# Kernel tuning notes

Measured on AMD Instinct MI355X. Metric: run time of the kernel, lower is better.

Reference implementation:

```python
import jax, jax.numpy as jnp
import numpy as np

MEAN = jnp.array([0.4488, 0.4371, 0.404], dtype=jnp.float32)
PS, PM, PL = 1e-4, 2e-4, 3e-4  # per-branch time costs ps/pm/pl
PATCH = 32
FACTOR = 4
GROUPS = 4


def _conv(x, w, b, pad, groups=1):
    y = jax.lax.conv_general_dilated(x, w, (1, 1), [(pad, pad), (pad, pad)],
                                     dimension_numbers=('NCHW', 'OIHW', 'NCHW'),
                                     feature_group_count=groups)
    return y + b[None, :, None, None]


def _block(x, w1, b1, w2, b2):
    # residual grouped-conv Block(channels, group=4)
    y = jax.nn.relu(_conv(x, w1, b1, 1, groups=GROUPS))
    return x + _conv(y, w2, b2, 1, groups=GROUPS)


def _pixel_shuffle(x, r):
    B, C, H, W = x.shape
    x = x.reshape(B, C // (r * r), r, r, H, W)
    return x.transpose(0, 1, 4, 2, 5, 3).reshape(B, C // (r * r), H * r, W * r)


def setup_inputs() -> dict:
    key = jax.random.key(0)
    ks = jax.random.split(key, 20)
    def W(i, shape, fan):
        return jax.random.normal(ks[i], shape, jnp.float32) * (fan ** -0.5)
    Z = lambda c: jnp.zeros((c,), jnp.float32)
    return {
        'x': jax.random.uniform(ks[0], (4, 3, 160, 160), dtype=jnp.float32),
        'tl': jnp.full((1,), 0.1, jnp.float32),
        'tr': jnp.full((1,), 0.1, jnp.float32),
        'iicm_w': W(1, (12, 3, 3, 3), 27), 'iicm_b': Z(12),
        'conv4_w': W(2, (64, 12, 3, 3), 108), 'conv4_b': Z(64),
        'b1_w1': W(3, (64, 16, 3, 3), 144), 'b1_b1': Z(64),
        'b1_w2': W(4, (64, 16, 3, 3), 144), 'b1_b2': Z(64),
        'c1_w': W(5, (64, 128, 1, 1), 128), 'c1_b': Z(64),
        'b2_w1': W(6, (64, 16, 3, 3), 144), 'b2_b1': Z(64),
        'b2_w2': W(7, (64, 16, 3, 3), 144), 'b2_b2': Z(64),
        'c2_w': W(8, (64, 192, 1, 1), 192), 'c2_b': Z(64),
        'b3_w1': W(9, (64, 16, 3, 3), 144), 'b3_b1': Z(64),
        'b3_w2': W(10, (64, 16, 3, 3), 144), 'b3_b2': Z(64),
        'c3_w': W(11, (64, 256, 1, 1), 256), 'c3_b': Z(64),
        'marm_w': W(12, (64, 67, 3, 3), 603), 'marm_b': Z(64),
        'up1_w': W(13, (256, 64, 3, 3), 576), 'up1_b': Z(256),
        'up2_w': W(14, (256, 64, 3, 3), 576), 'up2_b': Z(256),
        'upc_w': W(15, (3, 64, 3, 3), 576), 'upc_b': Z(3),
    }


def reference(x, tl, tr, iicm_w, iicm_b, conv4_w, conv4_b,
              b1_w1, b1_b1, b1_w2, b1_b2, c1_w, c1_b,
              b2_w1, b2_b1, b2_w2, b2_b2, c2_w, c2_b,
              b3_w1, b3_b1, b3_w2, b3_b2, c3_w, c3_b,
              marm_w, marm_b, up1_w, up1_b, up2_w, up2_b, upc_w, upc_b):
    # ----- sub_mean -----
    x0 = x - MEAN[None, :, None, None]
    B, C, H, W = x0.shape
    hp, wp = H // PATCH, W // PATCH
    N = B * hp * wp
    # ----- decompsition_img: tile into 32x32 patches -----
    p = x0.reshape(B, C, hp, PATCH, wp, PATCH).transpose(0, 2, 4, 1, 3, 5)
    p = p.reshape(N, C, PATCH, PATCH)
    # ----- IICM: feature extraction + per-patch difficulty score ssza -----
    f = jax.nn.relu(_conv(p, iicm_w, iicm_b, 1))          # [N,12,32,32]
    ssza = jnp.mean(jnp.abs(f), axis=(1, 2, 3))           # [N]
    f = _conv(f, conv4_w, conv4_b, 1)                     # [N,64,32,32]
    # ----- branch depth 1 -----
    b1o = _block(f, b1_w1, b1_b1, b1_w2, b1_b2)
    c1o = jnp.concatenate([f, b1o], axis=1)               # [N,128,...]
    xs_ = jax.nn.relu(_conv(c1o, c1_w, c1_b, 0))          # [N,64,...]
    # ----- branch depth 2 (original computes on non-routed subset; per-patch
    # convs are independent so dense compute + mask-select is the same math) --
    b2o = _block(xs_, b2_w1, b2_b1, b2_w2, b2_b2)
    c2o = jnp.concatenate([c1o, b2o], axis=1)             # [N,192,...]
    xm_ = jax.nn.relu(_conv(c2o, c2_w, c2_b, 0))
    # ----- branch depth 3 -----
    b3o = _block(xm_, b3_w1, b3_b1, b3_w2, b3_b2)
    c3o = jnp.concatenate([c2o, b3o], axis=1)             # [N,256,...]
    xh_ = jax.nn.relu(_conv(c3o, c3_w, c3_b, 0))
    # ----- threshold routing (mode 'test'): ssza vs tl, tl+tr -----
    tl0, tr0 = tl[0], tr[0]
    thr = tl0 + tr0
    m1 = ssza > thr                      # easy -> 1 block
    m2 = (ssza >= tl0) & (ssza <= thr)   # medium -> 2 blocks
    sel = lambda m, a, b: jnp.where(m[:, None, None, None], a, b)
    xout = sel(m1, xs_, sel(m2, xm_, xh_))                # [N,64,32,32]
    t = jnp.where(m1, PS * (ssza - thr),
                  jnp.where(m2, PM * tr0, PL * (tl0 - ssza)))
    timep = t.reshape(B, hp * wp).mean(axis=1, keepdims=True)  # [B,1]
    # ----- combination_img: stitch patches back -----
    feat = xout.reshape(B, hp, wp, 64, PATCH, PATCH).transpose(0, 3, 1, 4, 2, 5)
    feat = feat.reshape(B, 64, H, W)
    # ----- xcropia: per-patch activity mask at HR scale (channel 0 std) -----
    s = jnp.std(p[:, 0], axis=(1, 2))                     # [N]
    smap = jnp.broadcast_to(s[:, None, None], (N, PATCH, PATCH))
    smap = smap.reshape(B, hp, wp, PATCH, PATCH).transpose(0, 1, 3, 2, 4)
    smap = smap.reshape(B, 1, H, W)
    xcropia = jnp.repeat(jnp.repeat(smap, FACTOR, axis=2), FACTOR, axis=3)
    y = jax.nn.relu(_conv(jnp.concatenate([x0, feat], axis=1), marm_w, marm_b, 1))
    y = jax.nn.relu(_pixel_shuffle(_conv(y, up1_w, up1_b, 1), 2))
    y = jax.nn.relu(_pixel_shuffle(_conv(y, up2_w, up2_b, 1), 2))
    y = _conv(y, upc_w, upc_b, 1) + MEAN[None, :, None, None]
    xoutputa = y * xcropia
    return (y, timep, xcropia, xoutputa)
```

## Files before the change

### kernel.cpp

```cpp
#include <hip/hip_runtime.h>
#include <hip/hip_bf16.h>

typedef __hip_bfloat16 bf16;
typedef __bf16 bf16x8 __attribute__((ext_vector_type(8)));
typedef float f32x4 __attribute__((ext_vector_type(4)));

#define MEAN0 0.4488f
#define MEAN1 0.4371f
#define MEAN2 0.4040f

__global__ void k_iicm(const float* __restrict__ x, const float* __restrict__ w,
                       const float* __restrict__ bias, float* __restrict__ out,
                       bf16* __restrict__ outN16){
  __shared__ __align__(16) float ws_[324];
  __shared__ float bs[12];
  for(int k=threadIdx.x;k<324;k+=256){ int t0=k/12, kk=k%12; ws_[k]=w[kk*27+t0]; }
  if(threadIdx.x<12) bs[threadIdx.x]=bias[threadIdx.x];
  __syncthreads();
  int idx = blockIdx.x*256+threadIdx.x;
  int pix = idx & 1023, n = idx >> 10;
  int i = pix>>5, j = pix&31;
  int pw = n%5, ph=(n/5)%5, bb=n/25;
  float acc[12];
  #pragma unroll
  for(int k=0;k<12;k++) acc[k]=bs[k];
  #pragma unroll
  for(int c=0;c<3;c++){
    const float* xb = x + ((bb*3+c)*160 + ph*32)*160 + pw*32;
    float mc = (c==0)?MEAN0:((c==1)?MEAN1:MEAN2);
    #pragma unroll
    for(int dy=-1;dy<=1;dy++){
      int ii=i+dy; if((unsigned)ii>=32u) continue;
      #pragma unroll
      for(int dx=-1;dx<=1;dx++){
        int jj=j+dx; if((unsigned)jj>=32u) continue;
        float v = xb[ii*160+jj]-mc;
        int t0 = c*9+(dy+1)*3+(dx+1);
        const float4* wv = (const float4*)&ws_[t0*12];
        float4 w0=wv[0], w1=wv[1], w2=wv[2];
        acc[0]+=v*w0.x; acc[1]+=v*w0.y; acc[2]+=v*w0.z; acc[3]+=v*w0.w;
        acc[4]+=v*w1.x; acc[5]+=v*w1.y; acc[6]+=v*w1.z; acc[7]+=v*w1.w;
        acc[8]+=v*w2.x; acc[9]+=v*w2.y; acc[10]+=v*w2.z; acc[11]+=v*w2.w;
      }
    }
  }
  float* ob = out + n*12288 + pix;
  #pragma unroll
  for(int k=0;k<12;k++){ acc[k]=fmaxf(acc[k],0.f); ob[k*1024]=acc[k]; }
  union{ float4 v; bf16 h[8]; } p0, p1;
  #pragma unroll
  for(int k=0;k<8;k++) p0.h[k]=__float2bfloat16(acc[k]);
  #pragma unroll
  for(int k=0;k<4;k++) p1.h[k]=__float2bfloat16(acc[8+k]);
  #pragma unroll
  for(int k=4;k<8;k++) p1.h[k]=__float2bfloat16(0.f);
  bf16* o16 = outN16 + (size_t)(n*1024+pix)*16;
  *(float4*)o16 = p0.v;
  *(float4*)(o16+8) = p1.v;
}

__global__ void k_red(const float* __restrict__ f12, const float* __restrict__ x,
                      float* __restrict__ scalp){
  int n = blockIdx.x, t = threadIdx.x;
  __shared__ float sh[256];
  float s=0.f;
  const float* fb = f12 + n*12288;
  for(int k=t;k<12288;k+=256) s += fabsf(fb[k]);
  sh[t]=s; __syncthreads();
  for(int o=128;o>0;o>>=1){ if(t<o) sh[t]+=sh[t+o]; __syncthreads(); }
  if(t==0) scalp[n]=sh[0]*(1.f/12288.f);
  __syncthreads();
  int pw=n%5, ph=(n/5)%5, bb=n/25;
  const float* xb = x + ((bb*3+0)*160 + ph*32)*160 + pw*32;
  float sm=0.f, sq=0.f;
  for(int k=t;k<1024;k+=256){ int i=k>>5,j=k&31; float v=xb[i*160+j]-MEAN0; sm+=v; sq+=v*v; }
  sh[t]=sm; __syncthreads();
  for(int o=128;o>0;o>>=1){ if(t<o) sh[t]+=sh[t+o]; __syncthreads(); }
  float smean = sh[0]*(1.f/1024.f);
  __syncthreads();
  sh[t]=sq; __syncthreads();
  for(int o=128;o>0;o>>=1){ if(t<o) sh[t]+=sh[t+o]; __syncthreads(); }
  if(t==0){ float var = sh[0]*(1.f/1024.f) - smean*smean; scalp[128+n]=sqrtf(fmaxf(var,0.f)); }
}

__global__ void k_w4prep(const float* __restrict__ w, bf16* __restrict__ wp4){
  int idx = blockIdx.x*256+threadIdx.x;
  if(idx>=10240) return;
  int tp = idx/2048; int r2 = idx&2047;
  int oc = r2>>5; int k = r2&31;
  int ks = k>>3, e = k&7;
  int tap = 2*tp + (ks>>1);
  int ic = (ks&1)*8 + e;
  float v = (tap<9 && ic<12) ? w[oc*108 + ic*9 + tap] : 0.f;
  wp4[idx] = __float2bfloat16(v);
}

__global__ __launch_bounds__(128,3) void k_conv4M(const bf16* __restrict__ in,
                        const bf16* __restrict__ wp4, const float* __restrict__ bias,
                        bf16* __restrict__ outN){
  __shared__ __align__(16) __bf16 sB[204*2*8];
  int tid=threadIdx.x, bid=blockIdx.x;
  int n=bid>>3, tile=bid&7, y0=tile*4;
  const bf16* ib = in + (size_t)n*16384;
  for(int cid=tid; cid<408; cid+=128){
    int p=cid>>1, c=cid&1;
    int r=p/34, cc=p-r*34;
    int gy=y0-1+r, gx=cc-1;
    float4 v={0.f,0.f,0.f,0.f};
    if((unsigned)gy<32u && (unsigned)gx<32u)
      v = *(const float4*)(ib + (size_t)((gy<<5)+gx)*16 + c*8);
    *(float4*)(&sB[(size_t)(p*2 + (c^(p&1)))*8]) = v;
  }
  __syncthreads();
  int w_=tid>>6, l=tid&63;
  int ks=l>>4, l15=l&15;
  int h=ks>>1, cb=ks&1;
  f32x4 acc[4][4];
  #pragma unroll
  for(int i=0;i<4;i++)
    #pragma unroll
    for(int j=0;j<4;j++) acc[i][j]=(f32x4){0.f,0.f,0.f,0.f};
  int pr[4], pc[4];
  #pragma unroll
  for(int fn=0;fn<4;fn++){ int npx=w_*64+fn*16+l15; pr[fn]=npx>>5; pc[fn]=npx&31; }
  #pragma unroll
  for(int tp=0;tp<5;tp++){
    bf16x8 afr[4];
    #pragma unroll
    for(int fm=0;fm<4;fm++)
      afr[fm] = *(const bf16x8*)(wp4 + (((size_t)(tp*64 + fm*16 + l15))*4 + ks)*8);
    #pragma unroll
    for(int fm=0;fm<4;fm++) asm volatile("" : "+v"(afr[fm]));
    const int t0=2*tp, t1=(2*tp+1>8)?8:(2*tp+1);
    int ty = h ? (t1/3) : (t0/3);
    int tx = h ? (t1%3) : (t0%3);
    #pragma unroll
    for(int fn=0;fn<4;fn++){
      int p = (pr[fn]+ty)*34 + pc[fn]+tx;
      bf16x8 b = *(const bf16x8*)(&sB[(size_t)(p*2 + (cb^(p&1)))*8]);
      #pragma unroll
      for(int fm=0;fm<4;fm++)
        acc[fm][fn] = __builtin_amdgcn_mfma_f32_16x16x32_bf16(afr[fm], b, acc[fm][fn], 0,0,0);
    }
  }
  bf16* ob = outN + (size_t)n*65536;
  #pragma unroll
  for(int fm=0;fm<4;fm++){
    int oc0 = fm*16 + ks*4;
    #pragma unroll
    for(int fn=0;fn<4;fn++){
      int pxl = (y0+pr[fn])*32 + pc[fn];
      union{ uint2 u; bf16 hh[4]; } pk;
      #pragma unroll
      for(int j=0;j<4;j++) pk.hh[j]=__float2bfloat16(acc[fm][fn][j]+bias[oc0+j]);
      *(uint2*)(ob + (size_t)pxl*64 + oc0) = pk.u;
    }
  }
}

__global__ void k_wgprep2(const float* __restrict__ w0, const float* __restrict__ w1,
                          const float* __restrict__ w2, const float* __restrict__ w3,
                          const float* __restrict__ w4, const float* __restrict__ w5,
                          bf16* __restrict__ wpg){
  int idx = blockIdx.x*256+threadIdx.x;
  if(idx>=61440) return;
  int conv = idx/10240; int r = idx - conv*10240;
  int tp = r/2048; int r2 = r&2047;
  int oc = r2>>5; int k = r2&31;
  int ks = k>>3, e = k&7;
  int tap = 2*tp + (ks>>1);
  int il = (ks&1)*8 + e;
  const float* w = (conv==0)?w0:(conv==1)?w1:(conv==2)?w2:(conv==3)?w3:(conv==4)?w4:w5;
  float v = (tap<9) ? w[oc*144 + il*9 + tap] : 0.f;
  wpg[idx] = __float2bfloat16(v);
}

__global__ __launch_bounds__(128,3) void k_gconvM(const bf16* __restrict__ in,
                        const bf16* __restrict__ wg, const float* __restrict__ bias,
                        const bf16* __restrict__ resid, bf16* __restrict__ out, int do_relu){
  __shared__ __align__(16) __bf16 sB[204*8*8];
  int tid = threadIdx.x;
  int bid = blockIdx.x;
  int n = bid>>3, tile = bid&7;
  int y0 = tile*4;
  const bf16* ib = in + (size_t)n*65536;
  for(int cid=tid; cid<1632; cid+=128){
    int p = cid>>3, s = cid&7;
    int r = p/34, c = p - r*34;
    int gy = y0-1+r, gx = c-1;
    float4 v = {0.f,0.f,0.f,0.f};
    if((unsigned)gy<32u && (unsigned)gx<32u)
      v = *(const float4*)(ib + (size_t)((gy<<5)+gx)*64 + s*8);
    *(float4*)(&sB[(size_t)(p*8 + (s^(p&7)))*8]) = v;
  }
  __syncthreads();
  int w_ = tid>>6, l = tid&63;
  int ks = l>>4, l15 = l&15;
  int h = ks>>1, cb = ks&1;
  f32x4 acc[4][4];
  #pragma unroll
  for(int i=0;i<4;i++)
    #pragma unroll
    for(int j=0;j<4;j++) acc[i][j]=(f32x4){0.f,0.f,0.f,0.f};
  int pr[4], pc[4];
  #pragma unroll
  for(int fn=0;fn<4;fn++){ int npx = w_*64+fn*16+l15; pr[fn]=npx>>5; pc[fn]=npx&31; }
  #pragma unroll
  for(int tp=0;tp<5;tp++){
    bf16x8 afr[4];
    #pragma unroll
    for(int fm=0;fm<4;fm++)
      afr[fm] = *(const bf16x8*)(wg + (((size_t)(tp*64 + fm*16 + l15))*4 + ks)*8);
    #pragma unroll
    for(int fm=0;fm<4;fm++) asm volatile("" : "+v"(afr[fm]));
    const int t0=2*tp, t1=(2*tp+1>8)?8:(2*tp+1);
    int ty = h ? (t1/3) : (t0/3);
    int tx = h ? (t1%3) : (t0%3);
    #pragma unroll
    for(int fn=0;fn<4;fn++){
      int p = (pr[fn]+ty)*34 + pc[fn]+tx;
      int pb = p*8;
      #pragma unroll
      for(int fm=0;fm<4;fm++){
        int c = fm*2 + cb;
        bf16x8 b = *(const bf16x8*)(&sB[(size_t)(pb + (c^(p&7)))*8]);
        acc[fm][fn] = __builtin_amdgcn_mfma_f32_16x16x32_bf16(afr[fm], b, acc[fm][fn], 0,0,0);
      }
    }
  }
  bf16* ob = out + (size_t)n*65536;
  const bf16* rb = resid ? resid + (size_t)n*65536 : (const bf16*)0;
  #pragma unroll
  for(int fm=0;fm<4;fm++){
    int oc0 = fm*16 + ks*4;
    #pragma unroll
    for(int fn=0;fn<4;fn++){
      int pxl = (y0+pr[fn])*32 + pc[fn];
      float v[4];
      #pragma unroll
      for(int j=0;j<4;j++){
        float t = acc[fm][fn][j] + bias[oc0+j];
        if(do_relu) t = fmaxf(t,0.f);
        v[j]=t;
      }
      if(rb){
        union{ uint2 u; bf16 h[4]; } ru;
        ru.u = *(const uint2*)(rb + (size_t)pxl*64 + oc0);
        #pragma unroll
        for(int j=0;j<4;j++) v[j] += __bfloat162float(ru.h[j]);
      }
      union{ uint2 u; bf16 h[4]; } pk;
      #pragma unroll
      for(int j=0;j<4;j++) pk.h[j]=__float2bfloat16(v[j]);
      *(uint2*)(ob + (size_t)pxl*64 + oc0) = pk.u;
    }
  }
}

__global__ void k_wcprep(const float* __restrict__ w1, const float* __restrict__ w2,
                         const float* __restrict__ w3, bf16* __restrict__ wpc){
  int idx = blockIdx.x*256+threadIdx.x;
  const float* w; int Cin, base;
  if(idx<8192){ w=w1; Cin=128; base=0; }
  else if(idx<20480){ w=w2; Cin=192; base=8192; }
  else { w=w3; Cin=256; base=20480; }
  int r = idx-base;
  int g = r>>9, oc = (r>>3)&63, j = r&7;
  wpc[idx] = __float2bfloat16(w[oc*Cin + g*8 + j]);
}

__global__ __launch_bounds__(256,2) void k_1x1M(const bf16* __restrict__ s0,
                        const bf16* __restrict__ s1, const bf16* __restrict__ s2,
                        const bf16* __restrict__ s3, int ns,
                        const bf16* __restrict__ wpk, const float* __restrict__ bias,
                        bf16* __restrict__ outN){
  __shared__ __align__(16) __bf16 sA[32*64*8];
  __shared__ __align__(16) __bf16 sB[8*256*8];
  int tid = threadIdx.x;
  int px0 = blockIdx.x*256;
  for(int cid=tid; cid<ns*512; cid+=256)
    *(float4*)(&sA[(size_t)cid*8]) = ((const float4*)wpk)[cid];
  int w_ = tid>>6, l = tid&63;
  int ks = l>>4, l15 = l&15;
  f32x4 acc[4][4];
  #pragma unroll
  for(int i=0;i<4;i++)
    #pragma unroll
    for(int j=0;j<4;j++) acc[i][j]=(f32x4){0.f,0.f,0.f,0.f};
  const bf16* srcs[4]={s0,s1,s2,s3};
  for(int s=0;s<ns;s++){
    __syncthreads();
    const bf16* sp = srcs[s];
    #pragma unroll
    for(int it=0;it<8;it++){
      *(float4*)(&sB[(size_t)(it*256+tid)*8]) = *(const float4*)(sp + (size_t)(px0+tid)*64 + it*8);
    }
    __syncthreads();
    #pragma unroll
    for(int kk=0;kk<2;kk++){
      int tc = kk*4+ks;
      bf16x8 a[4], b[4];
      #pragma unroll
      for(int fm=0;fm<4;fm++) a[fm] = *(const bf16x8*)(&sA[(size_t)((s*8+tc)*64 + fm*16+l15)*8]);
      #pragma unroll
      for(int fn=0;fn<4;fn++) b[fn] = *(const bf16x8*)(&sB[(size_t)(tc*256 + w_*64+fn*16+l15)*8]);
      #pragma unroll
      for(int fm=0;fm<4;fm++)
        #pragma unroll
        for(int fn=0;fn<4;fn++)
          acc[fm][fn] = __builtin_amdgcn_mfma_f32_16x16x32_bf16(a[fm], b[fn], acc[fm][fn], 0,0,0);
    }
  }
  #pragma unroll
  for(int fm=0;fm<4;fm++){
    int oc0 = fm*16 + ks*4;
    #pragma unroll
    for(int fn=0;fn<4;fn++){
      int pxt = px0 + w_*64 + fn*16 + l15;
      union{ uint2 u; bf16 h[4]; } pk;
      #pragma unroll
      for(int j=0;j<4;j++) pk.h[j]=__float2bfloat16(fmaxf(acc[fm][fn][j]+bias[oc0+j],0.f));
      *(uint2*)(outN + (size_t)pxt*64 + oc0) = pk.u;
    }
  }
}

__global__ void k_routeN(const bf16* __restrict__ xs, const bf16* __restrict__ xm,
                         const bf16* __restrict__ xh, const float* __restrict__ xseg,
                         const float* __restrict__ scalp, const float* __restrict__ tl,
                         const float* __restrict__ tr, bf16* __restrict__ featN, int npix){
  int idx = blockIdx.x*256+threadIdx.x;
  int c = idx%12; int px = idx/12;
  if(px >= npix) return;
  int b = px/25600; int rem = px - b*25600;
  int y = rem/160, xx = rem - y*160;
  int n = b*25 + (y>>5)*5 + (xx>>5);
  float sz = scalp[n];
  float tl0 = tl[0], tr0 = tr[0], thr = tl0+tr0;
  const bf16* src = (sz>thr) ? xs : ((sz>=tl0 && sz<=thr) ? xm : xh);
  uint4 v = make_uint4(0,0,0,0);
  if(c < 8){
    v = *(const uint4*)(src + ((size_t)n*1024 + ((y&31)<<5) + (xx&31))*64 + c*8);
  } else if(c == 8){
    union{ uint4 q; bf16 h[8]; } pk;
    pk.q = make_uint4(0,0,0,0);
    pk.h[0]=__float2bfloat16(xseg[(b*3+0)*25600 + rem]-MEAN0);
    pk.h[1]=__float2bfloat16(xseg[(b*3+1)*25600 + rem]-MEAN1);
    pk.h[2]=__float2bfloat16(xseg[(b*3+2)*25600 + rem]-MEAN2);
    v = pk.q;
  }
  *(uint4*)(featN + (size_t)px*96 + c*8) = v;
}

__global__ void k_timep(const float* __restrict__ scalp, const float* __restrict__ tl,
                        const float* __restrict__ tr, float* __restrict__ dtp){
  __shared__ float sh[64];
  int b=blockIdx.x, t=threadIdx.x;
  float tl0=tl[0], tr0=tr[0], thr=tl0+tr0;
  float v=0.f;
  if(t<25){
    float sz=scalp[b*25+t];
    v = (sz>thr) ? 1e-4f*(sz-thr) : ((sz>=tl0 && sz<=thr) ? 2e-4f*tr0 : 3e-4f*(tl0-sz));
  }
  sh[t]=v; __syncthreads();
  for(int o=32;o>0;o>>=1){ if(t<o) sh[t]+=sh[t+o]; __syncthreads(); }
  if(t==0) dtp[b]=sh[0]*(1.f/25.f);
}

__global__ void k_wprep(const float* __restrict__ w1, const float* __restrict__ w2,
                        bf16* __restrict__ wp){
  int idx = blockIdx.x*256+threadIdx.x;
  int conv = idx/147456; int r = idx - conv*147456;
  int tap = r>>14; int r2 = r&16383;
  int s   = (r2>>11)&7;
  int oc  = (r2>>3)&255;
  int j   = r2&7;
  int ic = s*8+j;
  const float* w = conv? w2 : w1;
  wp[idx] = __float2bfloat16(w[oc*576 + ic*9 + tap]);
}

__global__ void k_wmprep(const float* __restrict__ w, bf16* __restrict__ wpm){
  int idx = blockIdx.x*256+threadIdx.x;
  if(idx>=55296) return;
  int tap = idx/6144; int r = idx - tap*6144;
  int icg = r>>9; int oc = (r>>3)&63; int j = r&7;
  int ic = icg*8+j;
  float v = 0.f;
  if(ic<64)      v = w[oc*603 + (3+ic)*9 + tap];
  else if(ic<67) v = w[oc*603 + (ic-64)*9 + tap];
  wpm[idx] = __float2bfloat16(v);
}

__global__ void k_wuprep(const float* __restrict__ w, bf16* __restrict__ wpu){
  int idx = blockIdx.x*256+threadIdx.x;
  if(idx>=9216) return;
  int tap = idx>>10; int r = idx&1023;
  int tc = r>>7; int oc = (r>>3)&15; int j = r&7;
  int ic = tc*8+j;
  float v = (oc<3) ? w[oc*576 + ic*9 + tap] : 0.f;
  wpu[idx] = __float2bfloat16(v);
}

__global__ __launch_bounds__(256,2) void k_marmM(const bf16* __restrict__ featN,
                        const bf16* __restrict__ wpm, const float* __restrict__ bias,
                        bf16* __restrict__ outN){
  __shared__ __align__(16) __bf16 sB[12*340*8];
  __shared__ __align__(16) __bf16 sA[12*64*8];
  int bid = blockIdx.x;
  int img = bid/100; int t_ = bid - img*100;
  int y0 = (t_/5)*8, x0 = (t_%5)*32;
  int tid = threadIdx.x;
  const bf16* ib = featN + (size_t)img*25600*96;
  for(int cid=tid; cid<4080; cid+=256){
    int icg = cid/340, p = cid - icg*340;
    int r = p/34, cc = p - r*34;
    int gy = y0-1+r, gx = x0-1+cc;
    float4 v = {0.f,0.f,0.f,0.f};
    if((unsigned)gy<160u && (unsigned)gx<160u)
      v = *(const float4*)(ib + (size_t)(gy*160+gx)*96 + icg*8);
    *(float4*)(&sB[(size_t)(icg*340+p)*8]) = v;
  }
  for(int cid=tid; cid<768; cid+=256)
    *(float4*)(&sA[(size_t)cid*8]) = ((const float4*)wpm)[cid];
  __syncthreads();
  int w_ = tid>>6, l = tid&63;
  int ks = l>>4, l15 = l&15;
  f32x4 acc[4][4];
  #pragma unroll
  for(int i=0;i<4;i++)
    #pragma unroll
    for(int j=0;j<4;j++) acc[i][j]=(f32x4){0.f,0.f,0.f,0.f};
  int pr[4], pc[4];
  #pragma unroll
  for(int fn=0;fn<4;fn++){ int npx = w_*64+fn*16+l15; pr[fn]=npx>>5; pc[fn]=npx&31; }
  float4 pre[3];
  for(int tap=0;tap<9;tap++){
    if(tap<8){
      #pragma unroll
      for(int k=0;k<3;k++) pre[k] = ((const float4*)wpm)[(tap+1)*768 + k*256 + tid];
    }
    int ty=tap/3, tx=tap-ty*3;
    #pragma unroll
    for(int kk=0;kk<3;kk++){
      int tc = kk*4+ks;
      bf16x8 a[4], b[4];
      #pragma unroll
      for(int fm=0;fm<4;fm++) a[fm] = *(const bf16x8*)(&sA[(size_t)(tc*64 + fm*16+l15)*8]);
      #pragma unroll
      for(int fn=0;fn<4;fn++)
        b[fn] = *(const bf16x8*)(&sB[(size_t)(tc*340 + (pr[fn]+ty)*34 + pc[fn]+tx)*8]);
      #pragma unroll
      for(int fm=0;fm<4;fm++)
        #pragma unroll
        for(int fn=0;fn<4;fn++)
          acc[fm][fn] = __builtin_amdgcn_mfma_f32_16x16x32_bf16(a[fm], b[fn], acc[fm][fn], 0,0,0);
    }
    if(tap<8){
      __syncthreads();
      #pragma unroll
      for(int k=0;k<3;k++) ((float4*)sA)[k*256+tid] = pre[k];
      __syncthreads();
    }
  }
  bf16* ob = outN + (size_t)img*25600*64;
  #pragma unroll
  for(int fm=0;fm<4;fm++){
    int oc0 = fm*16 + ks*4;
    #pragma unroll
    for(int fn=0;fn<4;fn++){
      int px = (y0+pr[fn])*160 + x0+pc[fn];
      union{ uint2 u; bf16 h[4]; } pk;
      #pragma unroll
      for(int j=0;j<4;j++) pk.h[j]=__float2bfloat16(fmaxf(acc[fm][fn][j]+bias[oc0+j],0.f));
      *(uint2*)(ob + (size_t)px*64 + oc0) = pk.u;
    }
  }
}

template<int H, int W>
__global__ __launch_bounds__(256,3) void k_convup(const bf16* __restrict__ in,
                        const bf16* __restrict__ wp, const float* __restrict__ bias,
                        bf16* __restrict__ out){
  constexpr int TXC = W/16, TPB = (H/4)*TXC;
  __shared__ __align__(16) char smem[16384];
  __bf16* sB = (__bf16*)smem;
  int bid = blockIdx.x;
  int img = bid/TPB; int t_ = bid - img*TPB;
  int y0 = (t_/TXC)*4, x0 = (t_%TXC)*16;
  int tid = threadIdx.x;
  const bf16* ib = in + (size_t)img*H*W*64;
  for(int cid=tid; cid<864; cid+=256){
    int p = cid>>3, tt = cid&7;
    int r = p/18, cc = p - r*18;
    int gy = y0-1+r, gx = x0-1+cc;
    float4 v = {0.f,0.f,0.f,0.f};
    if((unsigned)gy<(unsigned)H && (unsigned)gx<(unsigned)W)
      v = *(const float4*)(ib + ((size_t)(gy*W+gx)*64 + tt*8));
    *(float4*)(&sB[(size_t)(p*8 + (tt^(p&7)))*8]) = v;
  }
  __syncthreads();
  int w_ = tid>>6, l = tid&63;
  int ks = l>>4, l15 = l&15;
  f32x4 acc[4][4];
  #pragma unroll
  for(int i=0;i<4;i++)
    #pragma unroll
    for(int j=0;j<4;j++) acc[i][j]=(f32x4){0.f,0.f,0.f,0.f};
  const bf16* wpb = wp + ((size_t)w_*64 + l15)*8;
  #pragma unroll
  for(int kk=0;kk<2;kk++){
    int tc = kk*4+ks;
    #pragma unroll
    for(int tr=0;tr<3;tr++){
      bf16x8 afr[3][4];
      #pragma unroll
      for(int tx=0;tx<3;tx++)
        #pragma unroll
        for(int fm=0;fm<4;fm++)
          afr[tx][fm] = *(const bf16x8*)(wpb + ((size_t)(((tr*3+tx)*8+tc)*256) + fm*16)*8);
      #pragma unroll
      for(int tx=0;tx<3;tx++)
        #pragma unroll
        for(int fm=0;fm<4;fm++)
          asm volatile("" : "+v"(afr[tx][fm]));
      #pragma unroll
      for(int tx=0;tx<3;tx++){
        bf16x8 b[4];
        #pragma unroll
        for(int fn=0;fn<4;fn++){
          int p = (fn+tr)*18 + l15+tx;
          b[fn] = *(const bf16x8*)(&sB[(size_t)(p*8 + (tc^(p&7)))*8]);
        }
        #pragma unroll
        for(int fm=0;fm<4;fm++)
          #pragma unroll
          for(int fn=0;fn<4;fn++)
            acc[fm][fn] = __builtin_amdgcn_mfma_f32_16x16x32_bf16(afr[tx][fm], b[fn], acc[fm][fn], 0,0,0);
      }
    }
  }
  bf16* ob = out + (size_t)img*4*H*W*64;
  const int W2 = 2*W;
  char* oT = smem;
  #pragma unroll
  for(int h=0;h<2;h++){
    __syncthreads();
    #pragma unroll
    for(int fm=0;fm<4;fm++){
      int co = w_*16 + fm*4 + ks;
      #pragma unroll
      for(int j=0;j<4;j++){
        float bsv = bias[w_*64 + fm*16 + ks*4 + j];
        int r1=(j>>1)&1, r2=j&1;
        #pragma unroll
        for(int ff=0;ff<2;ff++){
          int fn = 2*h+ff;
          int opx = (2*ff+r1)*32 + 2*l15+r2;
          float v = fmaxf(acc[fm][fn][j]+bsv, 0.f);
          int sl = (co>>3) ^ ((opx>>1)&7);
          *(bf16*)(oT + opx*128 + sl*16 + (co&7)*2) = __float2bfloat16(v);
        }
      }
    }
    __syncthreads();
    #pragma unroll
    for(int k=0;k<4;k++){
      int cid = k*256 + tid;
      int p = cid>>3, lq = cid&7;
      int sl = lq ^ ((p>>1)&7);
      uint4 v = *(const uint4*)(oT + p*128 + sl*16);
      int Y = 2*y0 + 4*h + (p>>5), X = 2*x0 + (p&31);
      *(uint4*)(ob + ((size_t)Y*W2 + X)*64 + lq*8) = v;
    }
  }
}

__global__ __launch_bounds__(256,3) void k_upcM(const bf16* __restrict__ in,
                        const bf16* __restrict__ wpu, const float* __restrict__ bias,
                        const float* __restrict__ scal, float* __restrict__ dout, int b){
  __shared__ __align__(16) __bf16 sB[396*64];
  int tid = threadIdx.x;
  int t_ = blockIdx.x;
  int by0 = (t_/10)*4, bx0 = (t_%10)*64;
  for(int cid=tid; cid<3168; cid+=256){
    int px = cid>>3, c = cid&7;
    int hr = px/66, hc = px - hr*66;
    int gy = by0-1+hr, gx = bx0-1+hc;
    float4 v = {0.f,0.f,0.f,0.f};
    if((unsigned)gy<640u && (unsigned)gx<640u)
      v = *(const float4*)(in + ((size_t)(gy*640+gx))*64 + c*8);
    int slot = c ^ (px&7);
    *(float4*)(&sB[(size_t)px*64 + slot*8]) = v;
  }
  int w_ = tid>>6, l = tid&63;
  int ks = l>>4, l15 = l&15;
  bf16x8 afr[9][2];
  #pragma unroll
  for(int tap=0;tap<9;tap++)
    #pragma unroll
    for(int kk=0;kk<2;kk++)
      afr[tap][kk] = *(const bf16x8*)(wpu + (size_t)((tap*8 + kk*4+ks)*16 + l15)*8);
  __syncthreads();
  f32x4 acc[4];
  #pragma unroll
  for(int fn=0;fn<4;fn++) acc[fn]=(f32x4){0.f,0.f,0.f,0.f};
  int r = w_;
  int cxc[4];
  #pragma unroll
  for(int fn=0;fn<4;fn++) cxc[fn]=fn*16+l15;
  for(int tap=0;tap<9;tap++){
    int ty=tap/3, tx=tap-ty*3;
    #pragma unroll
    for(int kk=0;kk<2;kk++){
      int tc = kk*4+ks;
      #pragma unroll
      for(int fn=0;fn<4;fn++){
        int ph = (r+ty)*66 + cxc[fn]+tx;
        int slot = tc ^ (ph&7);
        bf16x8 bb = *(const bf16x8*)(&sB[(size_t)ph*64 + slot*8]);
        acc[fn] = __builtin_amdgcn_mfma_f32_16x16x32_bf16(afr[tap][kk], bb, acc[fn], 0,0,0);
      }
    }
  }
  if(ks==0){
    float c0=bias[0]+MEAN0, c1=bias[1]+MEAN1, c2=bias[2]+MEAN2;
    int gy = by0 + r;
    size_t yb=(size_t)b*3*409600;
    #pragma unroll
    for(int fn=0;fn<4;fn++){
      int gx = bx0 + cxc[fn];
      float a0=acc[fn][0]+c0, a1=acc[fn][1]+c1, a2=acc[fn][2]+c2;
      int n=b*25+(gy>>7)*5+(gx>>7);
      float sv=scal[128+n];
      size_t pidx=(size_t)gy*640+gx;
      dout[yb+pidx]=a0; dout[yb+409600+pidx]=a1; dout[yb+819200+pidx]=a2;
      dout[4915204 + (size_t)b*409600 + pidx]=sv;
      size_t xa=6553604+yb;
      dout[xa+pidx]=a0*sv; dout[xa+409600+pidx]=a1*sv; dout[xa+819200+pidx]=a2*sv;
    }
  }
}

extern "C" void kernel_launch(void* const* d_in, const int* in_sizes, int n_in,
                              void* d_out, int out_size, void* d_ws, size_t ws_size,
                              hipStream_t stream){
  const float* x     =(const float*)d_in[0];
  const float* tl    =(const float*)d_in[1];
  const float* tr    =(const float*)d_in[2];
  const float* iicm_w=(const float*)d_in[3];
  const float* iicm_b=(const float*)d_in[4];
  const float* conv4_w=(const float*)d_in[5];
  const float* conv4_b=(const float*)d_in[6];
  const float* b1_w1 =(const float*)d_in[7];  const float* b1_b1=(const float*)d_in[8];
  const float* b1_w2 =(const float*)d_in[9];  const float* b1_b2=(const float*)d_in[10];
  const float* c1_w  =(const float*)d_in[11]; const float* c1_b =(const float*)d_in[12];
  const float* b2_w1 =(const float*)d_in[13]; const float* b2_b1=(const float*)d_in[14];
  const float* b2_w2 =(const float*)d_in[15]; const float* b2_b2=(const float*)d_in[16];
  const float* c2_w  =(const float*)d_in[17]; const float* c2_b =(const float*)d_in[18];
  const float* b3_w1 =(const float*)d_in[19]; const float* b3_b1=(const float*)d_in[20];
  const float* b3_w2 =(const float*)d_in[21]; const float* b3_b2=(const float*)d_in[22];
  const float* c3_w  =(const float*)d_in[23]; const float* c3_b =(const float*)d_in[24];
  const float* marm_w=(const float*)d_in[25]; const float* marm_b=(const float*)d_in[26];
  const float* up1_w =(const float*)d_in[27]; const float* up1_b=(const float*)d_in[28];
  const float* up2_w =(const float*)d_in[29]; const float* up2_b=(const float*)d_in[30];
  const float* upc_w =(const float*)d_in[31]; const float* upc_b=(const float*)d_in[32];

  char* base = (char*)d_ws;
  float* out =(float*)d_out;
  float* scal=(float*)base;

  const int SEG = (ws_size >= 188417024ull) ? 4 : 1;
  const int NP  = SEG*25;
  const int NPix= NP*1024;

  const size_t F12 = (size_t)NP*49152;
  const size_t SZB = (size_t)NP*131072;
  float* f12 = (float*)(base + 1024);
  char* bufs = base + 1024 + F12;
  bf16* fN   = (bf16*)(bufs + 0*SZB);
  bf16* tmpN = (bf16*)(bufs + 1*SZB);
  bf16* xsN  = (bf16*)(bufs + 2*SZB);
  bf16* b1oN = (bf16*)(bufs + 3*SZB);
  bf16* b2oN = (bf16*)(bufs + 4*SZB);
  bf16* xmN  = (bf16*)(bufs + 5*SZB);
  bf16* b3oN = (bf16*)(bufs + 6*SZB);
  bf16* xhN  = (bf16*)(bufs + 7*SZB);
  bf16* featN= (bf16*)(bufs + 0*SZB);
  bf16* marmN= (bf16*)(bufs + 2*SZB);
  bf16* ps1  = (bf16*)(bufs + 4*SZB);
  bf16* ps2  = (bf16*)(bufs + 8*SZB);
  char* packs = bufs + 8*SZB + 52428800;
  bf16* wpc  = (bf16*)packs;
  bf16* wp1  = wpc + 36864;
  bf16* wp2  = wp1 + 147456;
  bf16* wpm  = wp2 + 147456;
  bf16* wpu  = wpm + 55296;
  bf16* wpg2 = wpu + 9216;
  bf16* wp4  = wpg2 + 61440;
  bf16* f16N = wp4 + 10240;

  k_wcprep<<<144, 256,0,stream>>>(c1_w, c2_w, c3_w, wpc);
  k_wprep <<<1152,256,0,stream>>>(up1_w, up2_w, wp1);
  k_wmprep<<<216, 256,0,stream>>>(marm_w, wpm);
  k_wuprep<<<36,  256,0,stream>>>(upc_w, wpu);
  k_wgprep2<<<240,256,0,stream>>>(b1_w1,b1_w2,b2_w1,b2_w2,b3_w1,b3_w2, wpg2);
  k_w4prep<<<40,  256,0,stream>>>(conv4_w, wp4);

  for(int b0=0;b0<4;b0+=SEG){
    int p0 = b0*25;
    const float* xseg = x + (size_t)b0*3*25600;
    float* scalp = scal + p0;

    k_iicm <<<NP*4,  256,0,stream>>>(xseg, iicm_w, iicm_b, f12, f16N);
    k_red  <<<NP,    256,0,stream>>>(f12, xseg, scalp);
    k_conv4M<<<NP*8, 128,0,stream>>>(f16N, wp4, conv4_b, fN);
    k_gconvM<<<NP*8, 128,0,stream>>>(fN,   wpg2,         b1_b1, (const bf16*)0, tmpN, 1);
    k_gconvM<<<NP*8, 128,0,stream>>>(tmpN, wpg2+10240,   b1_b2, fN,             b1oN, 0);
    k_1x1M <<<NP*4,  256,0,stream>>>(fN, b1oN, (const bf16*)0, (const bf16*)0, 2, wpc, c1_b, xsN);
    k_gconvM<<<NP*8, 128,0,stream>>>(xsN,  wpg2+2*10240, b2_b1, (const bf16*)0, tmpN, 1);
    k_gconvM<<<NP*8, 128,0,stream>>>(tmpN, wpg2+3*10240, b2_b2, xsN,            b2oN, 0);
    k_1x1M <<<NP*4,  256,0,stream>>>(fN, b1oN, b2oN, (const bf16*)0, 3, wpc+8192, c2_b, xmN);
    k_gconvM<<<NP*8, 128,0,stream>>>(xmN,  wpg2+4*10240, b3_b1, (const bf16*)0, tmpN, 1);
    k_gconvM<<<NP*8, 128,0,stream>>>(tmpN, wpg2+5*10240, b3_b2, xmN,            b3oN, 0);
    k_1x1M <<<NP*4,  256,0,stream>>>(fN, b1oN, b2oN, b3oN, 4, wpc+20480, c3_b, xhN);
    k_routeN<<<(NPix*12+255)/256,256,0,stream>>>(xsN, xmN, xhN, xseg, scalp, tl, tr, featN, NPix);
    k_timep<<<SEG,   64, 0,stream>>>(scalp, tl, tr, out + 4915200 + b0);
    k_marmM<<<SEG*100, 256,0,stream>>>(featN, wpm, marm_b, marmN);
    k_convup<160,160><<<SEG*400, 256,0,stream>>>(marmN, wp1, up1_b, ps1);
    for(int i=0;i<SEG;i++){
      k_convup<320,320><<<1600, 256,0,stream>>>(ps1 + (size_t)i*6553600, wp2, up2_b, ps2);
      k_upcM<<<1600,256,0,stream>>>(ps2, wpu, upc_b, scal, out, b0+i);
    }
  }
}
```

Measured before the change: 531.5 us.

## Merge weight-prep kernels, fuse reductions, batch upsample launches, drop f32 feature buffer

The six weight-packing kernels become one launch. The iicm kernel no longer writes the fp32 12-channel feature map; instead it emits per-block partial sums, so k_red reads only four partials. The timep reduction is folded into the routing kernel as extra blocks. The 1x1 kernel reads weights straight from global memory instead of staging them in LDS, with launch bounds raised to 4 blocks. The second upsample conv and upc now process two images per launch by writing to alternating buffers. The combined changes cut launch count and memory traffic, at the risk of ps2b aliasing the featN/fN buffer and some extra global weight reads.

```diff
diff --git a/kernel.cpp b/kernel.cpp
--- a/kernel.cpp
+++ b/kernel.cpp
@@ -10,10 +10,11 @@
 #define MEAN2 0.4040f
 
 __global__ void k_iicm(const float* __restrict__ x, const float* __restrict__ w,
-                       const float* __restrict__ bias, float* __restrict__ out,
-                       bf16* __restrict__ outN16){
+                       const float* __restrict__ bias, bf16* __restrict__ outN16,
+                       float* __restrict__ partial){
   __shared__ __align__(16) float ws_[324];
   __shared__ float bs[12];
+  __shared__ float sh[256];
   for(int k=threadIdx.x;k<324;k+=256){ int t0=k/12, kk=k%12; ws_[k]=w[kk*27+t0]; }
   if(threadIdx.x<12) bs[threadIdx.x]=bias[threadIdx.x];
   __syncthreads();
@@ -44,9 +45,9 @@
       }
     }
   }
-  float* ob = out + n*12288 + pix;
-  #pragma unroll
-  for(int k=0;k<12;k++){ acc[k]=fmaxf(acc[k],0.f); ob[k*1024]=acc[k]; }
+  float s=0.f;
+  #pragma unroll
+  for(int k=0;k<12;k++){ acc[k]=fmaxf(acc[k],0.f); s+=acc[k]; }
   union{ float4 v; bf16 h[8]; } p0, p1;
   #pragma unroll
   for(int k=0;k<8;k++) p0.h[k]=__float2bfloat16(acc[k]);
@@ -57,19 +58,17 @@
   bf16* o16 = outN16 + (size_t)(n*1024+pix)*16;
   *(float4*)o16 = p0.v;
   *(float4*)(o16+8) = p1.v;
-}
-
-__global__ void k_red(const float* __restrict__ f12, const float* __restrict__ x,
+  sh[threadIdx.x]=s; __syncthreads();
+  for(int o=128;o>0;o>>=1){ if(threadIdx.x<o) sh[threadIdx.x]+=sh[threadIdx.x+o]; __syncthreads(); }
+  if(threadIdx.x==0) partial[blockIdx.x]=sh[0];
+}
+
+__global__ void k_red(const float* __restrict__ partial, const float* __restrict__ x,
                       float* __restrict__ scalp){
   int n = blockIdx.x, t = threadIdx.x;
   __shared__ float sh[256];
-  float s=0.f;
-  const float* fb = f12 + n*12288;
-  for(int k=t;k<12288;k+=256) s += fabsf(fb[k]);
-  sh[t]=s; __syncthreads();
-  for(int o=128;o>0;o>>=1){ if(t<o) sh[t]+=sh[t+o]; __syncthreads(); }
-  if(t==0) scalp[n]=sh[0]*(1.f/12288.f);
-  __syncthreads();
+  if(t==0)
+    scalp[n] = (partial[n*4]+partial[n*4+1]+partial[n*4+2]+partial[n*4+3])*(1.f/12288.f);
   int pw=n%5, ph=(n/5)%5, bb=n/25;
   const float* xb = x + ((bb*3+0)*160 + ph*32)*160 + pw*32;
   float sm=0.f, sq=0.f;
@@ -83,16 +82,66 @@
   if(t==0){ float var = sh[0]*(1.f/1024.f) - smean*smean; scalp[128+n]=sqrtf(fmaxf(var,0.f)); }
 }
 
-__global__ void k_w4prep(const float* __restrict__ w, bf16* __restrict__ wp4){
+__global__ void k_wpack(const float* __restrict__ c1_w, const float* __restrict__ c2_w,
+                        const float* __restrict__ c3_w, const float* __restrict__ up1_w,
+                        const float* __restrict__ up2_w, const float* __restrict__ marm_w,
+                        const float* __restrict__ upc_w, const float* __restrict__ b1_w1,
+                        const float* __restrict__ b1_w2, const float* __restrict__ b2_w1,
+                        const float* __restrict__ b2_w2, const float* __restrict__ b3_w1,
+                        const float* __restrict__ b3_w2, const float* __restrict__ conv4_w,
+                        bf16* __restrict__ packs){
   int idx = blockIdx.x*256+threadIdx.x;
-  if(idx>=10240) return;
-  int tp = idx/2048; int r2 = idx&2047;
-  int oc = r2>>5; int k = r2&31;
-  int ks = k>>3, e = k&7;
-  int tap = 2*tp + (ks>>1);
-  int ic = (ks&1)*8 + e;
-  float v = (tap<9 && ic<12) ? w[oc*108 + ic*9 + tap] : 0.f;
-  wp4[idx] = __float2bfloat16(v);
+  if(idx>=467968) return;
+  float v;
+  if(idx<36864){
+    const float* w; int Cin, base;
+    if(idx<8192){ w=c1_w; Cin=128; base=0; }
+    else if(idx<20480){ w=c2_w; Cin=192; base=8192; }
+    else { w=c3_w; Cin=256; base=20480; }
+    int r=idx-base; int g=r>>9, oc=(r>>3)&63, j=r&7;
+    v = w[oc*Cin + g*8 + j];
+  } else if(idx<331776){
+    int r0=idx-36864;
+    int conv=r0/147456; int r=r0-conv*147456;
+    int tap=r>>14; int r2=r&16383;
+    int s=(r2>>11)&7, oc=(r2>>3)&255, j=r2&7;
+    int ic=s*8+j;
+    const float* w = conv? up2_w : up1_w;
+    v = w[oc*576 + ic*9 + tap];
+  } else if(idx<387072){
+    int r=idx-331776;
+    int tap=r/6144; int rr=r-tap*6144;
+    int icg=rr>>9, oc=(rr>>3)&63, j=rr&7;
+    int ic=icg*8+j;
+    v = 0.f;
+    if(ic<64)      v = marm_w[oc*603 + (3+ic)*9 + tap];
+    else if(ic<67) v = marm_w[oc*603 + (ic-64)*9 + tap];
+  } else if(idx<396288){
+    int r=idx-387072;
+    int tap=r>>10; int rr=r&1023;
+    int tc=rr>>7, oc=(rr>>3)&15, j=rr&7;
+    int ic=tc*8+j;
+    v = (oc<3) ? upc_w[oc*576 + ic*9 + tap] : 0.f;
+  } else if(idx<457728){
+    int r=idx-396288;
+    int conv=r/10240; int rr=r-conv*10240;
+    int tp=rr/2048; int r2=rr&2047;
+    int oc=r2>>5; int k=r2&31;
+    int ks=k>>3, e=k&7;
+    int tap=2*tp+(ks>>1);
+    int il=(ks&1)*8+e;
+    const float* w = (conv==0)?b1_w1:(conv==1)?b1_w2:(conv==2)?b2_w1:(conv==3)?b2_w2:(conv==4)?b3_w1:b3_w2;
+    v = (tap<9) ? w[oc*144 + il*9 + tap] : 0.f;
+  } else {
+    int r=idx-457728;
+    int tp=r/2048; int r2=r&2047;
+    int oc=r2>>5; int k=r2&31;
+    int ks=k>>3, e=k&7;
+    int tap=2*tp+(ks>>1);
+    int ic=(ks&1)*8+e;
+    v = (tap<9 && ic<12) ? conv4_w[oc*108 + ic*9 + tap] : 0.f;
+  }
+  packs[idx]=__float2bfloat16(v);
 }
 
 __global__ __launch_bounds__(128,3) void k_conv4M(const bf16* __restrict__ in,
@@ -156,23 +205,6 @@
       *(uint2*)(ob + (size_t)pxl*64 + oc0) = pk.u;
     }
   }
-}
-
-__global__ void k_wgprep2(const float* __restrict__ w0, const float* __restrict__ w1,
-                          const float* __restrict__ w2, const float* __restrict__ w3,
-                          const float* __restrict__ w4, const float* __restrict__ w5,
-                          bf16* __restrict__ wpg){
-  int idx = blockIdx.x*256+threadIdx.x;
-  if(idx>=61440) return;
-  int conv = idx/10240; int r = idx - conv*10240;
-  int tp = r/2048; int r2 = r&2047;
-  int oc = r2>>5; int k = r2&31;
-  int ks = k>>3, e = k&7;
-  int tap = 2*tp + (ks>>1);
-  int il = (ks&1)*8 + e;
-  const float* w = (conv==0)?w0:(conv==1)?w1:(conv==2)?w2:(conv==3)?w3:(conv==4)?w4:w5;
-  float v = (tap<9) ? w[oc*144 + il*9 + tap] : 0.f;
-  wpg[idx] = __float2bfloat16(v);
 }
 
 __global__ __launch_bounds__(128,3) void k_gconvM(const bf16* __restrict__ in,
@@ -257,29 +289,14 @@
   }
 }
 
-__global__ void k_wcprep(const float* __restrict__ w1, const float* __restrict__ w2,
-                         const float* __restrict__ w3, bf16* __restrict__ wpc){
-  int idx = blockIdx.x*256+threadIdx.x;
-  const float* w; int Cin, base;
-  if(idx<8192){ w=w1; Cin=128; base=0; }
-  else if(idx<20480){ w=w2; Cin=192; base=8192; }
-  else { w=w3; Cin=256; base=20480; }
-  int r = idx-base;
-  int g = r>>9, oc = (r>>3)&63, j = r&7;
-  wpc[idx] = __float2bfloat16(w[oc*Cin + g*8 + j]);
-}
-
-__global__ __launch_bounds__(256,2) void k_1x1M(const bf16* __restrict__ s0,
+__global__ __launch_bounds__(256,4) void k_1x1M(const bf16* __restrict__ s0,
                         const bf16* __restrict__ s1, const bf16* __restrict__ s2,
                         const bf16* __restrict__ s3, int ns,
                         const bf16* __restrict__ wpk, const float* __restrict__ bias,
                         bf16* __restrict__ outN){
-  __shared__ __align__(16) __bf16 sA[32*64*8];
   __shared__ __align__(16) __bf16 sB[8*256*8];
   int tid = threadIdx.x;
   int px0 = blockIdx.x*256;
-  for(int cid=tid; cid<ns*512; cid+=256)
-    *(float4*)(&sA[(size_t)cid*8]) = ((const float4*)wpk)[cid];
   int w_ = tid>>6, l = tid&63;
   int ks = l>>4, l15 = l&15;
   f32x4 acc[4][4];
@@ -301,7 +318,10 @@
       int tc = kk*4+ks;
       bf16x8 a[4], b[4];
       #pragma unroll
-      for(int fm=0;fm<4;fm++) a[fm] = *(const bf16x8*)(&sA[(size_t)((s*8+tc)*64 + fm*16+l15)*8]);
+      for(int fm=0;fm<4;fm++)
+        a[fm] = *(const bf16x8*)(wpk + ((size_t)((s*8+tc)*64 + fm*16+l15))*8);
+      #pragma unroll
+      for(int fm=0;fm<4;fm++) asm volatile("" : "+v"(a[fm]));
       #pragma unroll
       for(int fn=0;fn<4;fn++) b[fn] = *(const bf16x8*)(&sB[(size_t)(tc*256 + w_*64+fn*16+l15)*8]);
       #pragma unroll
@@ -325,18 +345,32 @@
   }
 }
 
-__global__ void k_routeN(const bf16* __restrict__ xs, const bf16* __restrict__ xm,
+__global__ void k_routeT(const bf16* __restrict__ xs, const bf16* __restrict__ xm,
                          const bf16* __restrict__ xh, const float* __restrict__ xseg,
                          const float* __restrict__ scalp, const float* __restrict__ tl,
-                         const float* __restrict__ tr, bf16* __restrict__ featN, int npix){
-  int idx = blockIdx.x*256+threadIdx.x;
+                         const float* __restrict__ tr, bf16* __restrict__ featN,
+                         int nroute, float* __restrict__ dtp){
+  __shared__ float sh[256];
+  int bidx = blockIdx.x;
+  float tl0 = tl[0], tr0 = tr[0], thr = tl0+tr0;
+  if(bidx >= nroute){
+    int b = bidx - nroute, t = threadIdx.x;
+    float v=0.f;
+    if(t<25){
+      float sz=scalp[b*25+t];
+      v = (sz>thr) ? 1e-4f*(sz-thr) : ((sz>=tl0 && sz<=thr) ? 2e-4f*tr0 : 3e-4f*(tl0-sz));
+    }
+    sh[t]=v; __syncthreads();
+    for(int o=128;o>0;o>>=1){ if(t<o) sh[t]+=sh[t+o]; __syncthreads(); }
+    if(t==0) dtp[b]=sh[0]*(1.f/25.f);
+    return;
+  }
+  int idx = bidx*256+threadIdx.x;
   int c = idx%12; int px = idx/12;
-  if(px >= npix) return;
   int b = px/25600; int rem = px - b*25600;
   int y = rem/160, xx = rem - y*160;
   int n = b*25 + (y>>5)*5 + (xx>>5);
   float sz = scalp[n];
-  float tl0 = tl[0], tr0 = tr[0], thr = tl0+tr0;
   const bf16* src = (sz>thr) ? xs : ((sz>=tl0 && sz<=thr) ? xm : xh);
   uint4 v = make_uint4(0,0,0,0);
   if(c < 8){
@@ -350,56 +384,6 @@
     v = pk.q;
   }
   *(uint4*)(featN + (size_t)px*96 + c*8) = v;
-}
-
-__global__ void k_timep(const float* __restrict__ scalp, const float* __restrict__ tl,
-                        const float* __restrict__ tr, float* __restrict__ dtp){
-  __shared__ float sh[64];
-  int b=blockIdx.x, t=threadIdx.x;
-  float tl0=tl[0], tr0=tr[0], thr=tl0+tr0;
-  float v=0.f;
-  if(t<25){
-    float sz=scalp[b*25+t];
-    v = (sz>thr) ? 1e-4f*(sz-thr) : ((sz>=tl0 && sz<=thr) ? 2e-4f*tr0 : 3e-4f*(tl0-sz));
-  }
-  sh[t]=v; __syncthreads();
-  for(int o=32;o>0;o>>=1){ if(t<o) sh[t]+=sh[t+o]; __syncthreads(); }
-  if(t==0) dtp[b]=sh[0]*(1.f/25.f);
-}
-
-__global__ void k_wprep(const float* __restrict__ w1, const float* __restrict__ w2,
-                        bf16* __restrict__ wp){
-  int idx = blockIdx.x*256+threadIdx.x;
-  int conv = idx/147456; int r = idx - conv*147456;
-  int tap = r>>14; int r2 = r&16383;
-  int s   = (r2>>11)&7;
-  int oc  = (r2>>3)&255;
-  int j   = r2&7;
-  int ic = s*8+j;
-  const float* w = conv? w2 : w1;
-  wp[idx] = __float2bfloat16(w[oc*576 + ic*9 + tap]);
-}
-
-__global__ void k_wmprep(const float* __restrict__ w, bf16* __restrict__ wpm){
-  int idx = blockIdx.x*256+threadIdx.x;
-  if(idx>=55296) return;
-  int tap = idx/6144; int r = idx - tap*6144;
-  int icg = r>>9; int oc = (r>>3)&63; int j = r&7;
-  int ic = icg*8+j;
-  float v = 0.f;
-  if(ic<64)      v = w[oc*603 + (3+ic)*9 + tap];
-  else if(ic<67) v = w[oc*603 + (ic-64)*9 + tap];
-  wpm[idx] = __float2bfloat16(v);
-}
-
-__global__ void k_wuprep(const float* __restrict__ w, bf16* __restrict__ wpu){
-  int idx = blockIdx.x*256+threadIdx.x;
-  if(idx>=9216) return;
-  int tap = idx>>10; int r = idx&1023;
-  int tc = r>>7; int oc = (r>>3)&15; int j = r&7;
-  int ic = tc*8+j;
-  float v = (oc<3) ? w[oc*576 + ic*9 + tap] : 0.f;
-  wpu[idx] = __float2bfloat16(v);
 }
 
 __global__ __launch_bounds__(256,2) void k_marmM(const bf16* __restrict__ featN,
@@ -480,8 +464,8 @@
 
 template<int H, int W>
 __global__ __launch_bounds__(256,3) void k_convup(const bf16* __restrict__ in,
-                        const bf16* __restrict__ wp, const float* __restrict__ bias,
-                        bf16* __restrict__ out){
+                        bf16* __restrict__ o0, bf16* __restrict__ o1,
+                        const bf16* __restrict__ wp, const float* __restrict__ bias){
   constexpr int TXC = W/16, TPB = (H/4)*TXC;
   __shared__ __align__(16) char smem[16384];
   __bf16* sB = (__bf16*)smem;
@@ -540,7 +524,7 @@
       }
     }
   }
-  bf16* ob = out + (size_t)img*4*H*W*64;
+  bf16* ob = ((img&1) ? o1 : o0) + (size_t)(img>>1)*((size_t)8*H*W*64);
   const int W2 = 2*W;
   char* oT = smem;
   #pragma unroll
@@ -576,12 +560,15 @@
   }
 }
 
-__global__ __launch_bounds__(256,3) void k_upcM(const bf16* __restrict__ in,
-                        const bf16* __restrict__ wpu, const float* __restrict__ bias,
-                        const float* __restrict__ scal, float* __restrict__ dout, int b){
+__global__ __launch_bounds__(256,3) void k_upcM(const bf16* __restrict__ i0,
+                        const bf16* __restrict__ i1, const bf16* __restrict__ wpu,
+                        const float* __restrict__ bias, const float* __restrict__ scal,
+                        float* __restrict__ dout, int b0){
   __shared__ __align__(16) __bf16 sB[396*64];
   int tid = threadIdx.x;
-  int t_ = blockIdx.x;
+  int img = blockIdx.x/1600; int t_ = blockIdx.x - img*1600;
+  const bf16* in = img ? i1 : i0;
+  int b = b0 + img;
   int by0 = (t_/10)*4, bx0 = (t_%10)*64;
   for(int cid=tid; cid<3168; cid+=256){
     int px = cid>>3, c = cid&7;
@@ -669,15 +656,14 @@
   char* base = (char*)d_ws;
   float* out =(float*)d_out;
   float* scal=(float*)base;
+  float* partial=(float*)(base+1024);
 
   const int SEG = (ws_size >= 188417024ull) ? 4 : 1;
   const int NP  = SEG*25;
   const int NPix= NP*1024;
 
-  const size_t F12 = (size_t)NP*49152;
   const size_t SZB = (size_t)NP*131072;
-  float* f12 = (float*)(base + 1024);
-  char* bufs = base + 1024 + F12;
+  char* bufs = base + 4096;
   bf16* fN   = (bf16*)(bufs + 0*SZB);
   bf16* tmpN = (bf16*)(bufs + 1*SZB);
   bf16* xsN  = (bf16*)(bufs + 2*SZB);
@@ -689,9 +675,10 @@
   bf16* featN= (bf16*)(bufs + 0*SZB);
   bf16* marmN= (bf16*)(bufs + 2*SZB);
   bf16* ps1  = (bf16*)(bufs + 4*SZB);
-  bf16* ps2  = (bf16*)(bufs + 8*SZB);
-  char* packs = bufs + 8*SZB + 52428800;
-  bf16* wpc  = (bf16*)packs;
+  bf16* ps2a = (bf16*)(bufs + 8*SZB);
+  bf16* ps2b = (bf16*)(bufs + 0*SZB);
+  char* packsp = bufs + 8*SZB + 52428800;
+  bf16* wpc  = (bf16*)packsp;
   bf16* wp1  = wpc + 36864;
   bf16* wp2  = wp1 + 147456;
   bf16* wpm  = wp2 + 147456;
@@ -700,20 +687,16 @@
   bf16* wp4  = wpg2 + 61440;
   bf16* f16N = wp4 + 10240;
 
-  k_wcprep<<<144, 256,0,stream>>>(c1_w, c2_w, c3_w, wpc);
-  k_wprep <<<1152,256,0,stream>>>(up1_w, up2_w, wp1);
-  k_wmprep<<<216, 256,0,stream>>>(marm_w, wpm);
-  k_wuprep<<<36,  256,0,stream>>>(upc_w, wpu);
-  k_wgprep2<<<240,256,0,stream>>>(b1_w1,b1_w2,b2_w1,b2_w2,b3_w1,b3_w2, wpg2);
-  k_w4prep<<<40,  256,0,stream>>>(conv4_w, wp4);
+  k_wpack<<<1829,256,0,stream>>>(c1_w,c2_w,c3_w, up1_w,up2_w, marm_w, upc_w,
+                                 b1_w1,b1_w2,b2_w1,b2_w2,b3_w1,b3_w2, conv4_w, wpc);
 
   for(int b0=0;b0<4;b0+=SEG){
     int p0 = b0*25;
     const float* xseg = x + (size_t)b0*3*25600;
     float* scalp = scal + p0;
 
-    k_iicm <<<NP*4,  256,0,stream>>>(xseg, iicm_w, iicm_b, f12, f16N);
-    k_red  <<<NP,    256,0,stream>>>(f12, xseg, scalp);
+    k_iicm <<<NP*4,  256,0,stream>>>(xseg, iicm_w, iicm_b, f16N, partial);
+    k_red  <<<NP,    256,0,stream>>>(partial, xseg, scalp);
     k_conv4M<<<NP*8, 128,0,stream>>>(f16N, wp4, conv4_b, fN);
     k_gconvM<<<NP*8, 128,0,stream>>>(fN,   wpg2,         b1_b1, (const bf16*)0, tmpN, 1);
     k_gconvM<<<NP*8, 128,0,stream>>>(tmpN, wpg2+10240,   b1_b2, fN,             b1oN, 0);
@@ -724,13 +707,14 @@
     k_gconvM<<<NP*8, 128,0,stream>>>(xmN,  wpg2+4*10240, b3_b1, (const bf16*)0, tmpN, 1);
     k_gconvM<<<NP*8, 128,0,stream>>>(tmpN, wpg2+5*10240, b3_b2, xmN,            b3oN, 0);
     k_1x1M <<<NP*4,  256,0,stream>>>(fN, b1oN, b2oN, b3oN, 4, wpc+20480, c3_b, xhN);
-    k_routeN<<<(NPix*12+255)/256,256,0,stream>>>(xsN, xmN, xhN, xseg, scalp, tl, tr, featN, NPix);
-    k_timep<<<SEG,   64, 0,stream>>>(scalp, tl, tr, out + 4915200 + b0);
+    k_routeT<<<NP*48+SEG,256,0,stream>>>(xsN, xmN, xhN, xseg, scalp, tl, tr, featN,
+                                         NP*48, out + 4915200 + b0);
     k_marmM<<<SEG*100, 256,0,stream>>>(featN, wpm, marm_b, marmN);
-    k_convup<160,160><<<SEG*400, 256,0,stream>>>(marmN, wp1, up1_b, ps1);
-    for(int i=0;i<SEG;i++){
-      k_convup<320,320><<<1600, 256,0,stream>>>(ps1 + (size_t)i*6553600, wp2, up2_b, ps2);
-      k_upcM<<<1600,256,0,stream>>>(ps2, wpu, upc_b, scal, out, b0+i);
-    }
-  }
-}
+    k_convup<160,160><<<SEG*400, 256,0,stream>>>(marmN, ps1, ps1 + 6553600, wp1, up1_b);
+    for(int i=0;i<SEG;i+=2){
+      int ni = (SEG-i>=2)?2:1;
+      k_convup<320,320><<<ni*1600, 256,0,stream>>>(ps1 + (size_t)i*6553600, ps2a, ps2b, wp2, up2_b);
+      k_upcM<<<ni*1600,256,0,stream>>>(ps2a, ps2b, wpu, upc_b, scal, out, b0+i);
+    }
+  }
+}
```

After: 464.5 us. 12.6% less time.
